# Optimization experiments

Measured on AMD Instinct MI355X. Metric: run time of the kernel, lower is better.

The kernel has to match this reference:

```python
import jax, jax.numpy as jnp
import numpy as np

B_, L, HID = 2, 1024, 2048
N, H, P, NA = 128, 64, 64, 32   # state, heads, head_dim, rope angle pairs
DIN = 2 * H * P + 2 * N + 3 * H + NA  # 8672
EPS = 1e-5
A_FLOOR = 1e-4


def setup_inputs() -> dict:
    key = jax.random.key(0)
    k0, k1, k2 = jax.random.split(key, 3)
    hidden_states = jax.random.normal(k0, (B_, L, HID), jnp.float32)
    in_proj_w = jax.random.normal(k1, (DIN, HID), jnp.float32) * 0.02
    out_proj_w = jax.random.normal(k2, (HID, H * P), jnp.float32) * 0.02
    # dt_bias init exactly as in the torch module
    rng = np.random.default_rng(0)
    dt = np.exp(rng.random(H) * (np.log(0.1) - np.log(0.001)) + np.log(0.001))
    dt = np.clip(dt, 1e-4, None)
    dt_bias = jnp.asarray(dt + np.log(-np.expm1(-dt)), jnp.float32)
    return {
        'hidden_states': hidden_states,
        'in_proj_w': in_proj_w,
        'dt_bias': dt_bias,
        'B_bias': jnp.ones((H, N), jnp.float32),
        'C_bias': jnp.ones((H, N), jnp.float32),
        'B_norm_w': jnp.ones((N,), jnp.float32),
        'C_norm_w': jnp.ones((N,), jnp.float32),
        'D': jnp.ones((H,), jnp.float32),
        'out_proj_w': out_proj_w,
    }


def _rmsnorm(x, w):
    var = jnp.mean(jnp.square(x), axis=-1, keepdims=True)
    return x * jax.lax.rsqrt(var + EPS) * w


def _forward(hidden_states, in_proj_w, dt_bias, B_bias, C_bias,
             B_norm_w, C_norm_w, D, out_proj_w):
    b, l, _ = hidden_states.shape
    proj = hidden_states @ in_proj_w.T  # (b,l,DIN)
    splits = np.cumsum([H * P, H * P, N, N, H, H, H])
    z, x, Braw, Craw, dd_dt, dd_A, trap, angles = jnp.split(proj, splits, axis=-1)
    z = z.reshape(b, l, H, P)
    x = x.reshape(b, l, H, P)
    # data-dependent A (per token, per head), clamped
    A = jnp.minimum(-jax.nn.softplus(dd_A.astype(jnp.float32)), -A_FLOOR)
    DT = jax.nn.softplus(dd_dt + dt_bias)          # (b,l,H)
    decay = jnp.exp(A * DT)                        # (b,l,H)
    lam = jax.nn.sigmoid(trap)                     # trapezoidal weight (b,l,H)
    # RMSNorm then per-head input-independent bias (n_groups=1, mimo_rank=1)
    Bn = _rmsnorm(Braw, B_norm_w)[:, :, None, :] + B_bias  # (b,l,H,N)
    Cn = _rmsnorm(Craw, C_norm_w)[:, :, None, :] + C_bias  # (b,l,H,N)
    # blockwise rotary on first 2*NA state dims, cumulative data-dependent phase
    phase = jnp.cumsum(angles[:, :, None, :].astype(jnp.float32) * DT[..., None], axis=1)  # (b,l,H,NA)
    cos, sin = jnp.cos(phase), jnp.sin(phase)

    def rope(v):
        v1, v2, rest = v[..., :NA], v[..., NA:2 * NA], v[..., 2 * NA:]
        return jnp.concatenate([v1 * cos - v2 * sin, v1 * sin + v2 * cos, rest], axis=-1)

    Bh = rope(Bn.astype(jnp.float32))
    Ch = rope(Cn.astype(jnp.float32))
    u = (x * DT[..., None]).astype(jnp.float32)    # (b,l,H,P)

    # selective scan with generalized trapezoidal discretization:
    # h_t = a_t h_{t-1} + (1-lam_t) u_t B_t^T + lam_t a_t u_{t-1} B_{t-1}^T
    def step(carry, inp):
        h, Gp = carry
        Bt, Ct, ut, dec, lm = inp
        G = ut[..., :, None] * Bt[..., None, :]    # (b,H,P,N)
        h = dec[..., None, None] * h + (1.0 - lm)[..., None, None] * G \
            + (lm * dec)[..., None, None] * Gp
        y = jnp.einsum('bhpn,bhn->bhp', h, Ct)
        return (h, G), y

    h0 = jnp.zeros((b, H, P, N), jnp.float32)
    xs = (Bh.transpose(1, 0, 2, 3), Ch.transpose(1, 0, 2, 3),
          u.transpose(1, 0, 2, 3), decay.transpose(1, 0, 2), lam.transpose(1, 0, 2))
    _, ys = jax.lax.scan(step, (h0, h0), xs)       # (l,b,H,P)
    y = ys.transpose(1, 0, 2, 3)
    y = y + D[None, None, :, None] * x             # skip connection
    y = y * jax.nn.silu(z)                         # output gate (Z path in kernel)
    y = y.reshape(b, l, H * P)
    return y @ out_proj_w.T


def reference(hidden_states, in_proj_w, dt_bias, B_bias, C_bias,
              B_norm_w, C_norm_w, D, out_proj_w):
    return _forward(hidden_states, in_proj_w, dt_bias, B_bias, C_bias,
                    B_norm_w, C_norm_w, D, out_proj_w)
```

## Files before the change

### kernel.cpp

```cpp
#include <hip/hip_runtime.h>
#include <hip/hip_bf16.h>
#include <cstdint>
#include <cstddef>

#define DEVINL __device__ __forceinline__

typedef __attribute__((ext_vector_type(8))) short bf16x8;
typedef __attribute__((ext_vector_type(4))) float f32x4;

DEVINL float bf2f(unsigned short u){
  union { unsigned u32; float f; } cv; cv.u32 = ((unsigned)u) << 16; return cv.f;
}
DEVINL unsigned short f2bf(float f){
  union { float f; unsigned u32; } cv; cv.f = f;
  unsigned u = cv.u32;
  return (unsigned short)((u + 0x7FFFu + ((u >> 16) & 1u)) >> 16);
}
DEVINL float softplusf(float x){ return x > 20.f ? x : log1pf(expf(x)); }

DEVINL void g2l16(const void* gptr, void* ldsptr){
  __builtin_amdgcn_global_load_lds(
      (const __attribute__((address_space(1))) unsigned int*)gptr,
      (__attribute__((address_space(3))) unsigned int*)(uintptr_t)ldsptr,
      16, 0, 0);
}

DEVINL int swzb(int row, int col){ return row*256 + ((col*2) ^ ((row&7)<<4)); }
DEVINL void ldsw_write8(unsigned short* b, int row, int col, bf16x8 v){
  *(bf16x8*)((char*)b + swzb(row,col)) = v;
}
DEVINL bf16x8 ldsw_read8(const unsigned short* b, int row, int col){
  return *(const bf16x8*)((const char*)b + swzb(row,col));
}
DEVINL void ldsw_write1(unsigned short* b, int row, int col, unsigned short v){
  *(unsigned short*)((char*)b + swzb(row,col)) = v;
}
DEVINL unsigned short ldsw_read1(const unsigned short* b, int row, int col){
  return *(const unsigned short*)((const char*)b + swzb(row,col));
}

DEVINL unsigned long long pack4(float4 v){
  return (unsigned long long)f2bf(v.x)
       | ((unsigned long long)f2bf(v.y) << 16)
       | ((unsigned long long)f2bf(v.z) << 32)
       | ((unsigned long long)f2bf(v.w) << 48);
}

__global__ __launch_bounds__(256) void k_conv3(
    const float* __restrict__ a, unsigned short* __restrict__ oa, int nba,
    const float* __restrict__ b, unsigned short* __restrict__ ob, int nbb,
    const float* __restrict__ c, unsigned short* __restrict__ oc)
{
  const float* in; unsigned short* out; long blk;
  if ((int)blockIdx.x < nba)            { in = a; out = oa; blk = blockIdx.x; }
  else if ((int)blockIdx.x < nba + nbb) { in = b; out = ob; blk = blockIdx.x - nba; }
  else                                  { in = c; out = oc; blk = blockIdx.x - nba - nbb; }
  long i = (blk * 256 + threadIdx.x) * 8;
  float4 v0 = *(const float4*)(in + i);
  float4 v1 = *(const float4*)(in + i + 4);
  unsigned long long pk[2] = { pack4(v0), pack4(v1) };
  *(bf16x8*)(out + i) = *(const bf16x8*)pk;
}

template<bool OUT_BF16, int BN>
__global__ __launch_bounds__(256) void k_gemm_bt(
    const unsigned short* __restrict__ A,
    const unsigned short* __restrict__ Bt,
    void* __restrict__ Cout,
    int K, int Nrows, int Npad, int xm, int tmx, int tnx)
{
  constexpr int NB = BN / 32;
  __shared__ unsigned short Asub[128*64];
  __shared__ unsigned short Bsub[BN*64];
  const int tid = threadIdx.x;
  const int x = blockIdx.x & 7, i = blockIdx.x >> 3;
  const int rt = (x % xm) * tmx + (i % tmx);
  const int ct = (x / xm) * tnx + (i / tmx);
  const int lane = tid & 63, wave = tid >> 6;
  const int wr = wave >> 1, wc = wave & 1;
  const int fr = lane & 15;
  const int fq = lane >> 4;

  const int srow0 = tid >> 3;
  const int sgrp  = (tid & 7) ^ ((tid >> 3) & 7);
  size_t aoff[4], boff[NB];
  #pragma unroll
  for (int j = 0; j < 4; j++){
    int row = j*32 + srow0;
    aoff[j] = (size_t)(rt*128 + row) * K + sgrp*8;
  }
  #pragma unroll
  for (int j = 0; j < NB; j++){
    int row = j*32 + srow0;
    int brow = ct*BN + row; if (brow > Nrows-1) brow = Nrows-1;
    boff[j] = (size_t)brow * K + sgrp*8;
  }

  f32x4 acc[4][NB] = {};

  for (int k0 = 0; k0 < K; k0 += 64){
    #pragma unroll
    for (int j = 0; j < 4; j++)
      g2l16(A + aoff[j] + k0, (char*)Asub + (j*256 + tid)*16);
    #pragma unroll
    for (int j = 0; j < NB; j++)
      g2l16(Bt + boff[j] + k0, (char*)Bsub + (j*256 + tid)*16);
    asm volatile("s_waitcnt vmcnt(0)" ::: "memory");
    __syncthreads();

    #pragma unroll
    for (int kk = 0; kk < 2; kk++){
      bf16x8 af[4], bfr[NB];
      const int slot = (kk*4 + fq) ^ (fr & 7);
      #pragma unroll
      for (int j = 0; j < 4; j++){
        int ra = wr*64 + j*16 + fr;
        af[j] = *(const bf16x8*)((const char*)Asub + ra*128 + slot*16);
      }
      #pragma unroll
      for (int j = 0; j < NB; j++){
        int rb = wc*(BN/2) + j*16 + fr;
        bfr[j] = *(const bf16x8*)((const char*)Bsub + rb*128 + slot*16);
      }
      #pragma unroll
      for (int mi = 0; mi < 4; mi++)
        #pragma unroll
        for (int ni = 0; ni < NB; ni++)
          acc[mi][ni] = __builtin_amdgcn_mfma_f32_16x16x32_bf16(af[mi], bfr[ni], acc[mi][ni], 0, 0, 0);
    }
    __syncthreads();
  }

  const int er = (lane >> 4) * 4;
  const int ec = lane & 15;
  #pragma unroll
  for (int mi = 0; mi < 4; mi++){
    #pragma unroll
    for (int ni = 0; ni < NB; ni++){
      const int row = rt*128 + wr*64 + mi*16 + er;
      const int col = ct*BN + wc*(BN/2) + ni*16 + ec;
      #pragma unroll
      for (int r = 0; r < 4; r++){
        if (OUT_BF16)
          ((unsigned short*)Cout)[(size_t)(row+r)*Npad + col] = f2bf(acc[mi][ni][r]);
        else
          ((float*)Cout)[(size_t)(row+r)*Npad + col] = acc[mi][ni][r];
      }
    }
  }
}

__global__ __launch_bounds__(512) void k_prep(
    const unsigned short* __restrict__ proj, const float* __restrict__ Bw,
    const float* __restrict__ Cw, const float* __restrict__ dtb,
    unsigned short* __restrict__ Bb2, unsigned short* __restrict__ Cb2,
    float* __restrict__ DTt, float* __restrict__ lamt,
    float* __restrict__ clcb, float* __restrict__ gb,
    unsigned short* __restrict__ cosb, unsigned short* __restrict__ sinb)
{
  const int tid = threadIdx.x;
  __shared__ float dtL[1024], lamL[1024];
  __shared__ float part[16][32];
  __shared__ float red[16];

  if (blockIdx.x >= 128){
    int row = (int)(blockIdx.x - 128)*4 + (tid >> 7);
    int n = tid & 127;
    size_t base = (size_t)row * 8704;
    float bv = bf2f(proj[base + 8192 + n]);
    float cv = bf2f(proj[base + 8320 + n]);
    float sb = bv*bv, sc = cv*cv;
    #pragma unroll
    for (int m = 1; m < 64; m <<= 1){ sb += __shfl_xor(sb, m, 64); sc += __shfl_xor(sc, m, 64); }
    int w = tid >> 6;
    if ((tid & 63) == 0){ red[w*2] = sb; red[w*2+1] = sc; }
    __syncthreads();
    int rw = (tid >> 7) * 2;
    sb = red[rw*2]   + red[rw*2+2];
    sc = red[rw*2+1] + red[rw*2+3];
    float rb = rsqrtf(sb*(1.f/128.f) + 1e-5f);
    float rc = rsqrtf(sc*(1.f/128.f) + 1e-5f);
    Bb2[row*128 + n] = f2bf(bv*rb*Bw[n]);
    Cb2[row*128 + n] = f2bf(cv*rc*Cw[n]);
    return;
  }

  const int bh = blockIdx.x, b = bh >> 6, h = bh & 63;
  const size_t sbase = (size_t)bh * 1024;
  const int lane = tid & 63;
  float ld0, ld1;
  {
    int l0 = tid*2;
    #pragma unroll
    for (int q = 0; q < 2; q++){
      int l = l0 + q;
      size_t pb = (size_t)(b*1024 + l) * 8704;
      float dd_dt = bf2f(proj[pb + 8448 + h]);
      float dd_A  = bf2f(proj[pb + 8512 + h]);
      float trap  = bf2f(proj[pb + 8576 + h]);
      float DT  = softplusf(dd_dt + dtb[h]);
      float A   = -fmaxf(softplusf(dd_A), 1e-4f);
      float lam = 1.f / (1.f + expf(-trap));
      dtL[l] = DT; lamL[l] = lam;
      if (q == 0) ld0 = A*DT; else ld1 = A*DT;
      DTt[sbase+l] = DT; lamt[sbase+l] = lam;
    }
  }
  __syncthreads();
  {
    float p1 = ld0 + ld1;
    float tot = p1;
    float incl = tot;
    #pragma unroll
    for (int off = 1; off < 64; off <<= 1){
      float u = __shfl_up(incl, off, 64);
      if (lane >= off) incl += u;
    }
    float excl = incl - tot;
    int l0 = tid*2;
    clcb[sbase+l0]   = excl + ld0;
    clcb[sbase+l0+1] = excl + p1;
    #pragma unroll
    for (int q = 0; q < 2; q++){
      int l = l0 + q;
      int ln = (l == 1023) ? 1023 : l + 1;
      gb[sbase+l] = 1.f - lamL[l] + lamL[ln];
    }
  }
  int na = tid & 31, c = tid >> 5;
  float s = 0.f;
  for (int q = 0; q < 64; q++){
    int l = c*64 + q; int row = b*1024 + l;
    float ang = bf2f(proj[(size_t)row*8704 + 8640 + na]);
    s = fmaf(ang, dtL[l], s);
  }
  part[c][na] = s;
  __syncthreads();
  float off = 0.f;
  for (int cc = 0; cc < c; cc++) off += part[cc][na];
  float ph = off;
  for (int q = 0; q < 64; q++){
    int l = c*64 + q; int row = b*1024 + l;
    float ang = bf2f(proj[(size_t)row*8704 + 8640 + na]);
    ph = fmaf(ang, dtL[l], ph);
    float sn, cs;
    __sincosf(ph, &sn, &cs);
    size_t o = ((size_t)row*64 + h)*32 + na;
    cosb[o] = f2bf(cs); sinb[o] = f2bf(sn);
  }
}

__global__ __launch_bounds__(512, 1) void k_intra(
    const unsigned short* __restrict__ proj,
    const unsigned short* __restrict__ Bb2, const unsigned short* __restrict__ Cb2,
    const float* __restrict__ Bbias, const float* __restrict__ Cbias,
    const unsigned short* __restrict__ cosb, const unsigned short* __restrict__ sinb,
    const float* __restrict__ DTt, const float* __restrict__ clcb,
    const float* __restrict__ gb, const float* __restrict__ lamt,
    const float* __restrict__ Dv, unsigned short* __restrict__ ybf,
    unsigned short* __restrict__ Gbuf)
{
  const int c = blockIdx.x & 7, bh = blockIdx.x >> 3;
  const int b = bh >> 6, h = bh & 63;
  const int tid = threadIdx.x, lane = tid & 63, wave = tid >> 6;
  const int wr = wave >> 2, wc = wave & 3;
  const int fr = lane & 15, fq = lane >> 4;

  __shared__ __align__(16) unsigned short Cs[128*128];
  __shared__ __align__(16) unsigned short Bs[128*128];
  __shared__ __align__(16) unsigned short BTs[128*128];
  __shared__ __align__(16) unsigned short Uts[64*128];
  __shared__ float clcs[128], lams[128], gs[128], wUs[128], dts[128];
  __shared__ float biasB[128], biasC[128];

  const int base = b*1024 + c*128;
  const size_t shbase = (size_t)bh * 1024;
  const float Dh = Dv[h];

  if (tid < 128){
    int l = c*128 + tid;
    clcs[tid] = clcb[shbase + l];
    dts[tid]  = DTt[shbase + l];
    lams[tid] = lamt[shbase + l];
    gs[tid]   = gb[shbase + l];
    biasB[tid] = Bbias[h*128 + tid];
  } else if (tid < 256){
    biasC[tid-128] = Cbias[h*128 + tid-128];
  }
  __syncthreads();
  if (tid < 128) wUs[tid] = __expf(clcs[127] - clcs[tid]) * gs[tid];

  {
    const int t = tid >> 2, q = tid & 3;
    const int grow = base + t;
    const size_t roff = (size_t)grow*128;
    if (q == 0){
      bf16x8 cc[4], sv[4];
      #pragma unroll
      for (int j = 0; j < 4; j++){
        cc[j] = *(const bf16x8*)(cosb + ((size_t)grow*64 + h)*32 + j*8);
        sv[j] = *(const bf16x8*)(sinb + ((size_t)grow*64 + h)*32 + j*8);
      }
      #pragma unroll
      for (int j = 0; j < 4; j++){
        bf16x8 vlo = *(const bf16x8*)(Cb2 + roff + j*8);
        bf16x8 vhi = *(const bf16x8*)(Cb2 + roff + 32 + j*8);
        bf16x8 olo, ohi;
        #pragma unroll
        for (int e = 0; e < 8; e++){
          float a = bf2f((unsigned short)vlo[e]) + biasC[j*8+e];
          float d = bf2f((unsigned short)vhi[e]) + biasC[32+j*8+e];
          float cf = bf2f((unsigned short)cc[j][e]);
          float sf = bf2f((unsigned short)sv[j][e]);
          olo[e] = (short)f2bf(a*cf - d*sf);
          ohi[e] = (short)f2bf(a*sf + d*cf);
        }
        ldsw_write8(Cs, t, j*8, olo);
        ldsw_write8(Cs, t, 32 + j*8, ohi);
      }
    } else if (q == 1){
      #pragma unroll
      for (int j = 0; j < 8; j++){
        bf16x8 v = *(const bf16x8*)(Cb2 + roff + 64 + j*8);
        bf16x8 o;
        #pragma unroll
        for (int e = 0; e < 8; e++) o[e] = (short)f2bf(bf2f((unsigned short)v[e]) + biasC[64+j*8+e]);
        ldsw_write8(Cs, t, 64 + j*8, o);
      }
    } else if (q == 2){
      bf16x8 cc[4], sv[4];
      #pragma unroll
      for (int j = 0; j < 4; j++){
        cc[j] = *(const bf16x8*)(cosb + ((size_t)grow*64 + h)*32 + j*8);
        sv[j] = *(const bf16x8*)(sinb + ((size_t)grow*64 + h)*32 + j*8);
      }
      #pragma unroll
      for (int j = 0; j < 4; j++){
        bf16x8 vlo = *(const bf16x8*)(Bb2 + roff + j*8);
        bf16x8 vhi = *(const bf16x8*)(Bb2 + roff + 32 + j*8);
        bf16x8 olo, ohi;
        #pragma unroll
        for (int e = 0; e < 8; e++){
          float a = bf2f((unsigned short)vlo[e]) + biasB[j*8+e];
          float d = bf2f((unsigned short)vhi[e]) + biasB[32+j*8+e];
          float cf = bf2f((unsigned short)cc[j][e]);
          float sf = bf2f((unsigned short)sv[j][e]);
          olo[e] = (short)f2bf(a*cf - d*sf);
          ohi[e] = (short)f2bf(a*sf + d*cf);
        }
        ldsw_write8(Bs, t, j*8, olo);
        ldsw_write8(Bs, t, 32 + j*8, ohi);
        #pragma unroll
        for (int e = 0; e < 8; e++){
          ldsw_write1(BTs, j*8+e, t, (unsigned short)olo[e]);
          ldsw_write1(BTs, 32+j*8+e, t, (unsigned short)ohi[e]);
        }
      }
    } else {
      #pragma unroll
      for (int j = 0; j < 8; j++){
        bf16x8 v = *(const bf16x8*)(Bb2 + roff + 64 + j*8);
        bf16x8 o;
        #pragma unroll
        for (int e = 0; e < 8; e++) o[e] = (short)f2bf(bf2f((unsigned short)v[e]) + biasB[64+j*8+e]);
        ldsw_write8(Bs, t, 64 + j*8, o);
        #pragma unroll
        for (int e = 0; e < 8; e++) ldsw_write1(BTs, 64+j*8+e, t, (unsigned short)o[e]);
      }
    }
  }
  {
    const int p = tid & 63, jg = tid >> 6;
    #pragma unroll 4
    for (int q = 0; q < 16; q++){
      int j = jg*16 + q;
      size_t pb = (size_t)(base + j) * 8704;
      float xx = bf2f(proj[pb + 4096 + h*64 + p]);
      ldsw_write1(Uts, p, j, f2bf(xx * dts[j]));
    }
  }
  __syncthreads();

  f32x4 acc1[4][2];
  #pragma unroll
  for (int mi = 0; mi < 4; mi++)
    #pragma unroll
    for (int ni = 0; ni < 2; ni++)
      acc1[mi][ni] = (f32x4){0.f,0.f,0.f,0.f};
  #pragma unroll
  for (int ks = 0; ks < 4; ks++){
    bf16x8 af[4], bj[2];
    #pragma unroll
    for (int mi = 0; mi < 4; mi++) af[mi] = ldsw_read8(Cs, wr*64+mi*16+fr, ks*32+fq*8);
    #pragma unroll
    for (int ni = 0; ni < 2; ni++) bj[ni] = ldsw_read8(Bs, wc*32+ni*16+fr, ks*32+fq*8);
    #pragma unroll
    for (int mi = 0; mi < 4; mi++)
      #pragma unroll
      for (int ni = 0; ni < 2; ni++)
        acc1[mi][ni] = __builtin_amdgcn_mfma_f32_16x16x32_bf16(af[mi], bj[ni], acc1[mi][ni], 0,0,0);
  }
  unsigned short pr[4][2][4];
  int jj[2]; float clcj[2], gj[2];
  #pragma unroll
  for (int ni = 0; ni < 2; ni++){ jj[ni] = wc*32+ni*16+fr; clcj[ni] = clcs[jj[ni]]; gj[ni] = gs[jj[ni]]; }
  #pragma unroll
  for (int mi = 0; mi < 4; mi++){
    #pragma unroll
    for (int r = 0; r < 4; r++){
      int t = wr*64+mi*16+fq*4+r;
      float ct_ = clcs[t], lt = lams[t];
      #pragma unroll
      for (int ni = 0; ni < 2; ni++){
        int j = jj[ni];
        float w = (j < t) ? __expf(ct_ - clcj[ni])*gj[ni] : ((j == t) ? (1.f - lt) : 0.f);
        pr[mi][ni][r] = f2bf(acc1[mi][ni][r] * w);
      }
    }
  }
  __syncthreads();
  #pragma unroll
  for (int mi = 0; mi < 4; mi++)
    #pragma unroll
    for (int ni = 0; ni < 2; ni++)
      #pragma unroll
      for (int r = 0; r < 4; r++)
        ldsw_write1(Bs, wr*64+mi*16+fq*4+r, wc*32+ni*16+fr, pr[mi][ni][r]);
  __syncthreads();

  f32x4 acc2[4];
  #pragma unroll
  for (int mi = 0; mi < 4; mi++) acc2[mi] = (f32x4){0.f,0.f,0.f,0.f};
  #pragma unroll
  for (int ks = 0; ks < 4; ks++){
    bf16x8 af[4], uj;
    #pragma unroll
    for (int mi = 0; mi < 4; mi++) af[mi] = ldsw_read8(Bs, wr*64+mi*16+fr, ks*32+fq*8);
    uj = ldsw_read8(Uts, wc*16+fr, ks*32+fq*8);
    #pragma unroll
    for (int mi = 0; mi < 4; mi++)
      acc2[mi] = __builtin_amdgcn_mfma_f32_16x16x32_bf16(af[mi], uj, acc2[mi], 0,0,0);
  }
  f32x4 accS[2][2];
  #pragma unroll
  for (int mi = 0; mi < 2; mi++)
    #pragma unroll
    for (int ni = 0; ni < 2; ni++)
      accS[mi][ni] = (f32x4){0.f,0.f,0.f,0.f};
  #pragma unroll
  for (int ks = 0; ks < 4; ks++){
    bf16x8 au[2], bn[2];
    #pragma unroll
    for (int mi = 0; mi < 2; mi++){
      bf16x8 raw = ldsw_read8(Uts, wr*32+mi*16+fr, ks*32+fq*8);
      #pragma unroll
      for (int e = 0; e < 8; e++){
        float f = bf2f((unsigned short)raw[e]) * wUs[ks*32+fq*8+e];
        au[mi][e] = (short)f2bf(f);
      }
    }
    #pragma unroll
    for (int ni = 0; ni < 2; ni++) bn[ni] = ldsw_read8(BTs, wc*32+ni*16+fr, ks*32+fq*8);
    #pragma unroll
    for (int mi = 0; mi < 2; mi++)
      #pragma unroll
      for (int ni = 0; ni < 2; ni++)
        accS[mi][ni] = __builtin_amdgcn_mfma_f32_16x16x32_bf16(au[mi], bn[ni], accS[mi][ni], 0,0,0);
  }

  #pragma unroll
  for (int mi = 0; mi < 4; mi++){
    #pragma unroll
    for (int r = 0; r < 4; r++){
      int t = wr*64+mi*16+fq*4+r;
      int p = wc*16+fr;
      float xv = bf2f(ldsw_read1(Uts, p, t)) / fmaxf(dts[t], 1e-30f);
      float o = acc2[mi][r] + Dh*xv;
      ybf[(size_t)(base + t)*4096 + h*64 + p] = f2bf(o);
    }
  }
  #pragma unroll
  for (int mi = 0; mi < 2; mi++)
    #pragma unroll
    for (int ni = 0; ni < 2; ni++)
      #pragma unroll
      for (int r = 0; r < 4; r++){
        int p = wr*32+mi*16+fq*4+r;
        int n = wc*32+ni*16+fr;
        Gbuf[(size_t)blockIdx.x*8192 + p*128 + n] = f2bf(accS[mi][ni][r]);
      }
}

__global__ __launch_bounds__(256) void k_scanstate(
    const float* __restrict__ clcb, unsigned short* __restrict__ Gbuf)
{
  const int bh = blockIdx.x, tid = threadIdx.x;
  float S[32];
  #pragma unroll
  for (int q = 0; q < 32; q++) S[q] = 0.f;
  const size_t gbase = (size_t)bh*65536 + (size_t)tid*32;
  for (int c = 0; c < 8; c++){
    float decEnd = __expf(clcb[(size_t)bh*1024 + c*128 + 127]);
    unsigned short* p = Gbuf + gbase + (size_t)c*8192;
    bf16x8 g[4], s[4];
    #pragma unroll
    for (int q = 0; q < 4; q++) g[q] = *(const bf16x8*)(p + q*8);
    #pragma unroll
    for (int q = 0; q < 4; q++)
      #pragma unroll
      for (int e = 0; e < 8; e++) s[q][e] = (short)f2bf(S[q*8+e]);
    #pragma unroll
    for (int q = 0; q < 4; q++) *(bf16x8*)(p + q*8) = s[q];
    #pragma unroll
    for (int q = 0; q < 4; q++)
      #pragma unroll
      for (int e = 0; e < 8; e++)
        S[q*8+e] = decEnd*S[q*8+e] + bf2f((unsigned short)g[q][e]);
  }
}

__global__ __launch_bounds__(256) void k_inter(
    const unsigned short* __restrict__ proj,
    const unsigned short* __restrict__ Cb2, const float* __restrict__ Cbias,
    const unsigned short* __restrict__ cosb, const unsigned short* __restrict__ sinb,
    const float* __restrict__ clcb, const unsigned short* __restrict__ Sprev,
    unsigned short* __restrict__ ybf,
    const float* __restrict__ wo, unsigned short* __restrict__ wobf)
{
  if (blockIdx.x >= 1024){
    long i = (((long)blockIdx.x - 1024) * 256 + threadIdx.x) * 4;
    float4 v = *(const float4*)(wo + i);
    *(unsigned long long*)(wobf + i) = pack4(v);
    return;
  }
  const int c = blockIdx.x & 7, bh = blockIdx.x >> 3;
  const int b = bh >> 6, h = bh & 63;
  const int tid = threadIdx.x, lane = tid & 63, wave = tid >> 6;
  const int wr = wave >> 1, wc = wave & 1;
  const int fr = lane & 15, fq = lane >> 4;

  __shared__ __align__(16) unsigned short Cs[128*128];
  __shared__ __align__(16) unsigned short Ss[64*128];
  __shared__ float expclcs[128], biasC[128];

  const int base = b*1024 + c*128;

  if (tid < 128){
    expclcs[tid] = __expf(clcb[(size_t)bh*1024 + c*128 + tid]);
    biasC[tid] = Cbias[h*128 + tid];
  }
  __syncthreads();

  {
    const int t = tid >> 1, half = tid & 1;
    const int grow = base + t;
    const size_t roff = (size_t)grow*128 + half*64;
    if (half == 0){
      bf16x8 cc[4], sv[4];
      #pragma unroll
      for (int j = 0; j < 4; j++){
        cc[j] = *(const bf16x8*)(cosb + ((size_t)grow*64 + h)*32 + j*8);
        sv[j] = *(const bf16x8*)(sinb + ((size_t)grow*64 + h)*32 + j*8);
      }
      #pragma unroll
      for (int j = 0; j < 4; j++){
        bf16x8 vlo = *(const bf16x8*)(Cb2 + roff + j*8);
        bf16x8 vhi = *(const bf16x8*)(Cb2 + roff + 32 + j*8);
        bf16x8 olo, ohi;
        #pragma unroll
        for (int e = 0; e < 8; e++){
          float a = bf2f((unsigned short)vlo[e]) + biasC[j*8+e];
          float d = bf2f((unsigned short)vhi[e]) + biasC[32+j*8+e];
          float cf = bf2f((unsigned short)cc[j][e]);
          float sf = bf2f((unsigned short)sv[j][e]);
          olo[e] = (short)f2bf(a*cf - d*sf);
          ohi[e] = (short)f2bf(a*sf + d*cf);
        }
        ldsw_write8(Cs, t, j*8, olo);
        ldsw_write8(Cs, t, 32 + j*8, ohi);
      }
    } else {
      #pragma unroll
      for (int j = 0; j < 8; j++){
        bf16x8 v = *(const bf16x8*)(Cb2 + roff + j*8);
        bf16x8 o;
        #pragma unroll
        for (int e = 0; e < 8; e++) o[e] = (short)f2bf(bf2f((unsigned short)v[e]) + biasC[64+j*8+e]);
        ldsw_write8(Cs, t, 64 + j*8, o);
      }
    }
  }
  {
    const unsigned short* src = Sprev + (size_t)blockIdx.x*8192 + (size_t)tid*32;
    #pragma unroll
    for (int j = 0; j < 4; j++){
      bf16x8 v = *(const bf16x8*)(src + j*8);
      int f = tid*32 + j*8;
      ldsw_write8(Ss, f >> 7, f & 127, v);
    }
  }
  __syncthreads();

  f32x4 acc[4][2];
  #pragma unroll
  for (int mi = 0; mi < 4; mi++)
    #pragma unroll
    for (int ni = 0; ni < 2; ni++)
      acc[mi][ni] = (f32x4){0.f,0.f,0.f,0.f};
  #pragma unroll
  for (int ks = 0; ks < 4; ks++){
    bf16x8 af[4], sj[2];
    #pragma unroll
    for (int mi = 0; mi < 4; mi++) af[mi] = ldsw_read8(Cs, wr*64+mi*16+fr, ks*32+fq*8);
    #pragma unroll
    for (int ni = 0; ni < 2; ni++) sj[ni] = ldsw_read8(Ss, wc*32+ni*16+fr, ks*32+fq*8);
    #pragma unroll
    for (int mi = 0; mi < 4; mi++)
      #pragma unroll
      for (int ni = 0; ni < 2; ni++)
        acc[mi][ni] = __builtin_amdgcn_mfma_f32_16x16x32_bf16(af[mi], sj[ni], acc[mi][ni], 0,0,0);
  }

  #pragma unroll
  for (int mi = 0; mi < 4; mi++){
    #pragma unroll
    for (int ni = 0; ni < 2; ni++){
      #pragma unroll
      for (int r = 0; r < 4; r++){
        int t = wr*64+mi*16+fq*4+r;
        int p = wc*32+ni*16+fr;
        size_t yoff = (size_t)(base + t)*4096 + h*64 + p;
        float y = bf2f(ybf[yoff]) + expclcs[t]*acc[mi][ni][r];
        float zv = bf2f(proj[(size_t)(base + t)*8704 + h*64 + p]);
        float sl = zv / (1.f + __expf(-zv));
        ybf[yoff] = f2bf(y * sl);
      }
    }
  }
}

extern "C" void kernel_launch(void* const* d_in, const int* in_sizes, int n_in,
                              void* d_out, int out_size, void* d_ws, size_t ws_size,
                              hipStream_t stream)
{
  const float* hs    = (const float*)d_in[0];
  const float* w1    = (const float*)d_in[1];
  const float* dtb   = (const float*)d_in[2];
  const float* Bbias = (const float*)d_in[3];
  const float* Cbias = (const float*)d_in[4];
  const float* Bw    = (const float*)d_in[5];
  const float* Cw    = (const float*)d_in[6];
  const float* Dv    = (const float*)d_in[7];
  const float* wo    = (const float*)d_in[8];
  float* out = (float*)d_out;
  char* ws = (char*)d_ws;

  unsigned short* projbf = (unsigned short*)(ws + 0UL);
  unsigned short* W1bf   = (unsigned short*)(ws + 35651584UL);
  unsigned short* Gbuf   = W1bf;
  unsigned short* ybf    = (unsigned short*)(ws + 52428800UL);
  unsigned short* hsbf   = (unsigned short*)(ws + 71172096UL);
  unsigned short* cosb   = hsbf;
  unsigned short* sinb   = (unsigned short*)(ws + 79560704UL);
  float* DTt    = (float*)(ws + 87949312UL);
  float* lamt   = (float*)(ws + 88997888UL);
  float* clcb   = (float*)(ws + 89522176UL);
  float* gb     = (float*)(ws + 90046464UL);
  unsigned short* Bb2 = (unsigned short*)(ws + 90570752UL);
  unsigned short* Cb2 = (unsigned short*)(ws + 91095040UL);
  if (ws_size < 91619328UL) return;

  const bool bigws = (ws_size >= 91619328UL + 16777216UL);
  unsigned short* Wobf = bigws ? (unsigned short*)(ws + 91619328UL) : W1bf;

  (void)in_sizes; (void)n_in; (void)out_size;

  k_conv3<<<bigws ? 14816 : 10720, 256, 0, stream>>>(
      w1, W1bf, 8672, hs, hsbf, 2048, wo, Wobf);
  k_gemm_bt<true, 128><<<1088, 256, 0, stream>>>(hsbf, W1bf, projbf, 2048, 8672, 8704, 2, 8, 17);
  k_prep<<<640, 512, 0, stream>>>(projbf, Bw, Cw, dtb, Bb2, Cb2,
                                  DTt, lamt, clcb, gb, cosb, sinb);
  k_intra<<<1024, 512, 0, stream>>>(projbf, Bb2, Cb2, Bbias, Cbias,
                                    cosb, sinb, DTt, clcb, gb, lamt, Dv, ybf, Gbuf);
  k_scanstate<<<128, 256, 0, stream>>>(clcb, Gbuf);
  k_inter<<<bigws ? 1024 : 9216, 256, 0, stream>>>(
      projbf, Cb2, Cbias, cosb, sinb, clcb, Gbuf, ybf, wo, Wobf);
  k_gemm_bt<false, 64><<<512, 256, 0, stream>>>(ybf, Wobf, out, 4096, 2048, 2048, 4, 4, 16);
}
```

Measured before the change: 310.1 us.

## Split-K the output projection GEMM and vectorize x loads in intra kernel

Replaces the 512-block output GEMM with a 1024-block split-K version. Each half covers K=2048, one half writes directly to the output and the other writes to a scratch partial buffer that reuses the proj workspace, and a small add kernel then sums the two. The goal is to fill more compute units on the 4096x2048x4096 GEMM, at the cost of an extra fp32 round trip plus one more launch. Separately, the intra kernel now loads x with 8-wide bf16 vector loads instead of scalar per-element loads.

```diff
diff --git a/kernel.cpp b/kernel.cpp
--- a/kernel.cpp
+++ b/kernel.cpp
@@ -148,6 +148,101 @@
       }
     }
   }
+}
+
+__global__ __launch_bounds__(256) void k_gemm2sk(
+    const unsigned short* __restrict__ A,
+    const unsigned short* __restrict__ Bt,
+    float* __restrict__ out, float* __restrict__ part)
+{
+  constexpr int K = 4096, BN = 64, NB = 2;
+  __shared__ unsigned short Asub[128*64];
+  __shared__ unsigned short Bsub[BN*64];
+  const int tid = threadIdx.x;
+  const int half = (int)(blockIdx.x >> 9);
+  const int bid  = (int)(blockIdx.x & 511);
+  const int kbeg = half * 2048;
+  float* dst = half ? part : out;
+  const int x = bid & 7, i = bid >> 3;
+  const int rt = (x % 4) * 4 + (i % 4);
+  const int ct = (x / 4) * 16 + (i / 4);
+  const int lane = tid & 63, wave = tid >> 6;
+  const int wr = wave >> 1, wc = wave & 1;
+  const int fr = lane & 15;
+  const int fq = lane >> 4;
+
+  const int srow0 = tid >> 3;
+  const int sgrp  = (tid & 7) ^ ((tid >> 3) & 7);
+  size_t aoff[4], boff[NB];
+  #pragma unroll
+  for (int j = 0; j < 4; j++){
+    int row = j*32 + srow0;
+    aoff[j] = (size_t)(rt*128 + row) * K + sgrp*8;
+  }
+  #pragma unroll
+  for (int j = 0; j < NB; j++){
+    int row = j*32 + srow0;
+    boff[j] = (size_t)(ct*BN + row) * K + sgrp*8;
+  }
+
+  f32x4 acc[4][NB] = {};
+
+  for (int k0 = kbeg; k0 < kbeg + 2048; k0 += 64){
+    #pragma unroll
+    for (int j = 0; j < 4; j++)
+      g2l16(A + aoff[j] + k0, (char*)Asub + (j*256 + tid)*16);
+    #pragma unroll
+    for (int j = 0; j < NB; j++)
+      g2l16(Bt + boff[j] + k0, (char*)Bsub + (j*256 + tid)*16);
+    asm volatile("s_waitcnt vmcnt(0)" ::: "memory");
+    __syncthreads();
+
+    #pragma unroll
+    for (int kk = 0; kk < 2; kk++){
+      bf16x8 af[4], bfr[NB];
+      const int slot = (kk*4 + fq) ^ (fr & 7);
+      #pragma unroll
+      for (int j = 0; j < 4; j++){
+        int ra = wr*64 + j*16 + fr;
+        af[j] = *(const bf16x8*)((const char*)Asub + ra*128 + slot*16);
+      }
+      #pragma unroll
+      for (int j = 0; j < NB; j++){
+        int rb = wc*(BN/2) + j*16 + fr;
+        bfr[j] = *(const bf16x8*)((const char*)Bsub + rb*128 + slot*16);
+      }
+      #pragma unroll
+      for (int mi = 0; mi < 4; mi++)
+        #pragma unroll
+        for (int ni = 0; ni < NB; ni++)
+          acc[mi][ni] = __builtin_amdgcn_mfma_f32_16x16x32_bf16(af[mi], bfr[ni], acc[mi][ni], 0, 0, 0);
+    }
+    __syncthreads();
+  }
+
+  const int er = (lane >> 4) * 4;
+  const int ec = lane & 15;
+  #pragma unroll
+  for (int mi = 0; mi < 4; mi++){
+    #pragma unroll
+    for (int ni = 0; ni < NB; ni++){
+      const int row = rt*128 + wr*64 + mi*16 + er;
+      const int col = ct*BN + wc*(BN/2) + ni*16 + ec;
+      #pragma unroll
+      for (int r = 0; r < 4; r++)
+        dst[(size_t)(row+r)*2048 + col] = acc[mi][ni][r];
+    }
+  }
+}
+
+__global__ __launch_bounds__(256) void k_addout(
+    float* __restrict__ out, const float* __restrict__ part)
+{
+  long i = ((long)blockIdx.x*256 + threadIdx.x) * 4;
+  float4 a = *(const float4*)(out + i);
+  float4 b = *(const float4*)(part + i);
+  a.x += b.x; a.y += b.y; a.z += b.z; a.w += b.w;
+  *(float4*)(out + i) = a;
 }
 
 __global__ __launch_bounds__(512) void k_prep(
@@ -370,13 +465,17 @@
     }
   }
   {
-    const int p = tid & 63, jg = tid >> 6;
-    #pragma unroll 4
-    for (int q = 0; q < 16; q++){
-      int j = jg*16 + q;
+    const int jr = tid >> 3;
+    const int p0 = (tid & 7) * 8;
+    #pragma unroll
+    for (int q = 0; q < 2; q++){
+      int j = q*64 + jr;
       size_t pb = (size_t)(base + j) * 8704;
-      float xx = bf2f(proj[pb + 4096 + h*64 + p]);
-      ldsw_write1(Uts, p, j, f2bf(xx * dts[j]));
+      bf16x8 v = *(const bf16x8*)(proj + pb + 4096 + h*64 + p0);
+      float dj = dts[j];
+      #pragma unroll
+      for (int e = 0; e < 8; e++)
+        ldsw_write1(Uts, p0+e, j, f2bf(bf2f((unsigned short)v[e]) * dj));
     }
   }
   __syncthreads();
@@ -656,6 +755,7 @@
   char* ws = (char*)d_ws;
 
   unsigned short* projbf = (unsigned short*)(ws + 0UL);
+  float* gemm2part       = (float*)(ws + 0UL);
   unsigned short* W1bf   = (unsigned short*)(ws + 35651584UL);
   unsigned short* Gbuf   = W1bf;
   unsigned short* ybf    = (unsigned short*)(ws + 52428800UL);
@@ -685,5 +785,6 @@
   k_scanstate<<<128, 256, 0, stream>>>(clcb, Gbuf);
   k_inter<<<bigws ? 1024 : 9216, 256, 0, stream>>>(
       projbf, Cb2, Cbias, cosb, sinb, clcb, Gbuf, ybf, wo, Wobf);
-  k_gemm_bt<false, 64><<<512, 256, 0, stream>>>(ybf, Wobf, out, 4096, 2048, 2048, 4, 4, 16);
-}
+  k_gemm2sk<<<1024, 256, 0, stream>>>(ybf, Wobf, out, gemm2part);
+  k_addout<<<4096, 256, 0, stream>>>(out, gemm2part);
+}
```

After: 298.5 us. 1.04x faster.
